# Performance work log

Measured on AMD Instinct MI355X. Metric: run time of the kernel, lower is better.

The kernel has to match this reference:

```python
import jax, jax.numpy as jnp
import numpy as np
from jax import lax

B, T, F, H = 128, 4096, 64, 128

def setup_inputs() -> dict:
    key = jax.random.key(0)
    k1, k2, k3, k4, k5 = jax.random.split(key, 5)
    s = 1.0 / np.sqrt(H)  # PyTorch LSTM init scale
    X = jax.random.normal(k1, (B, T, F), dtype=jnp.float32)
    W_ih = jax.random.uniform(k2, (4 * H, F), minval=-s, maxval=s, dtype=jnp.float32)
    W_hh = jax.random.uniform(k3, (4 * H, H), minval=-s, maxval=s, dtype=jnp.float32)
    b_ih = jax.random.uniform(k4, (4 * H,), minval=-s, maxval=s, dtype=jnp.float32)
    b_hh = jax.random.uniform(k5, (4 * H,), minval=-s, maxval=s, dtype=jnp.float32)
    return {"X": X, "W_ih": W_ih, "W_hh": W_hh, "b_ih": b_ih, "b_hh": b_hh}

def reference(X, W_ih, W_hh, b_ih, b_hh):
    # Faithful to the torch module: per-sequence LSTM with zero init state,
    # returning the output at the final timestep (== final hidden state).
    # PyTorch gate order: i, f, g, o.
    Bn, Tn, _ = X.shape
    Hn = W_hh.shape[1]
    # Precompute input contribution for all timesteps: [B, T, 4H]
    xg = jnp.einsum('btf,gf->btg', X, W_ih) + b_ih + b_hh
    xg_t = jnp.swapaxes(xg, 0, 1)  # [T, B, 4H]

    def step(carry, xg_step):
        h, c = carry
        gates = xg_step + h @ W_hh.T  # [B, 4H]
        i, f, g, o = jnp.split(gates, 4, axis=-1)
        i = jax.nn.sigmoid(i)
        f = jax.nn.sigmoid(f)
        g = jnp.tanh(g)
        o = jax.nn.sigmoid(o)
        c = f * c + i * g
        h = o * jnp.tanh(c)
        return (h, c), None

    h0 = jnp.zeros((Bn, Hn), dtype=X.dtype)
    c0 = jnp.zeros((Bn, Hn), dtype=X.dtype)
    (h_last, _), _ = lax.scan(step, (h0, c0), xg_t)
    return h_last  # [B, H]: the torch code's list of (1,1,H) outs, stacked
```

## Files before the change

### kernel.cpp

```cpp
#include <hip/hip_runtime.h>

#define B_  128
#define T_  4096
#define F_  64
#define H_  128
#define NT  512
#define XGS 516

typedef _Float16 half8_t __attribute__((ext_vector_type(8)));
typedef _Float16 half2_t __attribute__((ext_vector_type(2)));
typedef float    f32x4   __attribute__((ext_vector_type(4)));

#define L2N1 (-1.4426950408889634f)
#define L2N2 (-2.8853900817779268f)

__device__ __forceinline__ half2_t pack2(float a, float b) {
  half2_t r; r[0] = (_Float16)a; r[1] = (_Float16)b; return r;
}

__device__ __forceinline__ void wg_barrier() {
  __asm__ volatile("s_waitcnt lgkmcnt(0)\n\ts_barrier" ::: "memory");
}

__global__ __launch_bounds__(NT, 2) void lstm_xg_kernel(
    const float* __restrict__ X,
    const float* __restrict__ Wih,
    const float* __restrict__ Whh,
    const float* __restrict__ bih,
    const float* __restrict__ bhh,
    float* __restrict__ out)
{
  const int tid  = threadIdx.x;
  const int b    = blockIdx.x;
  const int lane = tid & 63;
  const int w    = tid >> 6;
  const int lg   = lane >> 4;
  const int lc   = lane & 15;

  __shared__ __align__(16) _Float16 hbuf[2][H_];
  __shared__ __align__(16) _Float16 xst[2][16 * 72];
  __shared__ __align__(16) float    xg[2][16 * XGS];

  half8_t Wf[4][6];
  f32x4   xinit[4];
#pragma unroll
  for (int g = 0; g < 4; ++g) {
    const float s = (g == 2) ? L2N2 : L2N1;
    const int row = 128 * g + 16 * w + lc;
    const float bv = (bih[row] + bhh[row]) * s;
    f32x4 bi = {bv, bv, bv, bv};
    xinit[g] = bi;
#pragma unroll
    for (int c = 0; c < 6; ++c) {
      const float* src = (c < 4) ? (Whh + (size_t)row * H_ + 32 * c + 8 * lg)
                                 : (Wih + (size_t)row * F_ + 32 * (c - 4) + 8 * lg);
      float4 lo = *(const float4*)(src);
      float4 hi = *(const float4*)(src + 4);
      half8_t v;
      v[0] = (_Float16)(lo.x * s); v[1] = (_Float16)(lo.y * s);
      v[2] = (_Float16)(lo.z * s); v[3] = (_Float16)(lo.w * s);
      v[4] = (_Float16)(hi.x * s); v[5] = (_Float16)(hi.y * s);
      v[6] = (_Float16)(hi.z * s); v[7] = (_Float16)(hi.w * s);
      Wf[g][c] = v;
    }
  }

  const float* xbase = X + (size_t)b * T_ * F_;
  const int    tp    = tid >> 5;
  const int    kp    = tid & 31;

  {
    float2 v0 = ((const float2*)xbase)[0 * 512 + tid];
    float2 v1 = ((const float2*)xbase)[1 * 512 + tid];
    *(half2_t*)&xst[0][tp * 72 + 2 * kp] = pack2(v0.x, v0.y);
    *(half2_t*)&xst[1][tp * 72 + 2 * kp] = pack2(v1.x, v1.y);
  }
  wg_barrier();

  const f32x4 zf = {0.0f, 0.0f, 0.0f, 0.0f};

  {
    half8_t a0 = *(const half8_t*)&xst[0][lc * 72 + 8 * lg];
    half8_t a1 = *(const half8_t*)&xst[0][lc * 72 + 32 + 8 * lg];
#pragma unroll
    for (int g = 0; g < 4; ++g) {
      f32x4 ab = __builtin_amdgcn_mfma_f32_16x16x32_f16(a0, Wf[g][4], xinit[g], 0, 0, 0);
      ab       = __builtin_amdgcn_mfma_f32_16x16x32_f16(a1, Wf[g][5], ab, 0, 0, 0);
#pragma unroll
      for (int r = 0; r < 4; ++r)
        xg[0][(4 * lg + r) * XGS + (16 * w + lc) * 4 + g] = ab[r];
    }
  }
  wg_barrier();

  f32x4 pre[4], pB[4];
#pragma unroll
  for (int g = 0; g < 4; ++g) { pre[g] = zf; pB[g] = zf; }
  f32x4 xg4 = *(const f32x4*)&xg[0][0 * XGS + (16 * w + lc) * 4];

  float csS = 0.0f, hl = 0.0f;
  float2 xv = {0.0f, 0.0f};

#pragma unroll 16
  for (int t = 0; t < T_; ++t) {
    const int buf = t & 1;
    const int P   = t >> 4;
    const int tau = t & 15;

    float p0 = pre[0][0] + pB[0][0] + xg4[0];
    float p1 = pre[1][0] + pB[1][0] + xg4[1];
    float p2 = pre[2][0] + pB[2][0] + xg4[2];
    float p3 = pre[3][0] + pB[3][0] + xg4[3];

    float si = __builtin_amdgcn_rcpf(1.0f + __builtin_amdgcn_exp2f(p0));
    float sf = __builtin_amdgcn_rcpf(1.0f + __builtin_amdgcn_exp2f(p1));
    float rg = __builtin_amdgcn_rcpf(1.0f + __builtin_amdgcn_exp2f(p2));
    float so = __builtin_amdgcn_rcpf(1.0f + __builtin_amdgcn_exp2f(p3));

    float ai = si * L2N2;
    csS = fmaf(sf, csS, fmaf(ai + ai, rg, -ai));

    float so2 = so + so, son = -so;
    float rh  = __builtin_amdgcn_rcpf(1.0f + __builtin_amdgcn_exp2f(csS));
    float hn  = fmaf(so2, rh, son);
    hl = hn;

    if (lane < 16) hbuf[buf][16 * w + lc] = (_Float16)hn;

    wg_barrier();

    half8_t ah0 = *(const half8_t*)&hbuf[buf][ 0 + 8 * lg];
    half8_t ah1 = *(const half8_t*)&hbuf[buf][32 + 8 * lg];
    half8_t ah2 = *(const half8_t*)&hbuf[buf][64 + 8 * lg];
    half8_t ah3 = *(const half8_t*)&hbuf[buf][96 + 8 * lg];

    const int tn = t + 1;
    xg4 = *(const f32x4*)&xg[(tn >> 4) & 1][(tn & 15) * XGS + (16 * w + lc) * 4];

    if (tau == 0) {
      const int sb = (P + 1) & 1;
      half8_t a0 = *(const half8_t*)&xst[sb][lc * 72 + 8 * lg];
      half8_t a1 = *(const half8_t*)&xst[sb][lc * 72 + 32 + 8 * lg];
#pragma unroll
      for (int g = 0; g < 4; ++g) {
        f32x4 ab = __builtin_amdgcn_mfma_f32_16x16x32_f16(a0, Wf[g][4], xinit[g], 0, 0, 0);
        ab       = __builtin_amdgcn_mfma_f32_16x16x32_f16(a1, Wf[g][5], ab, 0, 0, 0);
#pragma unroll
        for (int r = 0; r < 4; ++r)
          xg[sb][(4 * lg + r) * XGS + (16 * w + lc) * 4 + g] = ab[r];
      }
      int Pn = P + 2; if (Pn > (T_ / 16 - 1)) Pn = T_ / 16 - 1;
      xv = ((const float2*)xbase)[(size_t)Pn * 512 + tid];
    }
    if (tau == 8) {
      *(half2_t*)&xst[P & 1][tp * 72 + 2 * kp] = pack2(xv.x, xv.y);
    }

#pragma unroll
    for (int g = 0; g < 4; ++g) {
      f32x4 a  = __builtin_amdgcn_mfma_f32_16x16x32_f16(ah0, Wf[g][0], zf, 0, 0, 0);
      pre[g]   = __builtin_amdgcn_mfma_f32_16x16x32_f16(ah1, Wf[g][1], a, 0, 0, 0);
      f32x4 a2 = __builtin_amdgcn_mfma_f32_16x16x32_f16(ah2, Wf[g][2], zf, 0, 0, 0);
      pB[g]    = __builtin_amdgcn_mfma_f32_16x16x32_f16(ah3, Wf[g][3], a2, 0, 0, 0);
    }
  }

  if (lane < 16) out[(size_t)b * H_ + 16 * w + lc] = hl;
}

extern "C" void kernel_launch(void* const* d_in, const int* in_sizes, int n_in,
                              void* d_out, int out_size, void* d_ws, size_t ws_size,
                              hipStream_t stream) {
  const float* X   = (const float*)d_in[0];
  const float* Wih = (const float*)d_in[1];
  const float* Whh = (const float*)d_in[2];
  const float* bih = (const float*)d_in[3];
  const float* bhh = (const float*)d_in[4];
  float* out = (float*)d_out;

  lstm_xg_kernel<<<dim3(B_), dim3(NT), 0, stream>>>(X, Wih, Whh, bih, bhh, out);
}
```

Baseline: 1.860 ms.

## Split LSTM gate activations across wave halves and stagger input projection MFMAs

Each wave half now computes only two of the four gate nonlinearities (lanes below 32 handle i and g, lanes 32 and up handle f and o). The i*g term is exchanged with a cross-half shuffle, which shortens the serial transcendental chain per timestep. The xg layout is permuted so each half reads a float2 instead of a float4. The per-chunk input-projection MFMAs are split across two timesteps (tau 0 and 1) to spread that load, at the cost of an extra shuffle on the critical path and keeping xa0/xa1 live in registers.

New measurement: 2.001 ms. 7.6% more time.

```diff
diff --git a/kernel.cpp b/kernel.cpp
--- a/kernel.cpp
+++ b/kernel.cpp
@@ -13,6 +13,10 @@
 
 #define L2N1 (-1.4426950408889634f)
 #define L2N2 (-2.8853900817779268f)
+
+__device__ __forceinline__ constexpr int gslot(int g) {
+  return (g & 1) ? (2 + (g >> 1)) : (g >> 1);
+}
 
 __device__ __forceinline__ half2_t pack2(float a, float b) {
   half2_t r; r[0] = (_Float16)a; r[1] = (_Float16)b; return r;
@@ -36,6 +40,7 @@
   const int w    = tid >> 6;
   const int lg   = lane >> 4;
   const int lc   = lane & 15;
+  const bool hi32 = lane >= 32;
 
   __shared__ __align__(16) _Float16 hbuf[2][H_];
   __shared__ __align__(16) _Float16 xst[2][16 * 72];
@@ -88,7 +93,7 @@
       ab       = __builtin_amdgcn_mfma_f32_16x16x32_f16(a1, Wf[g][5], ab, 0, 0, 0);
 #pragma unroll
       for (int r = 0; r < 4; ++r)
-        xg[0][(4 * lg + r) * XGS + (16 * w + lc) * 4 + g] = ab[r];
+        xg[0][(4 * lg + r) * XGS + (16 * w + lc) * 4 + gslot(g)] = ab[r];
     }
   }
   wg_barrier();
@@ -96,10 +101,11 @@
   f32x4 pre[4], pB[4];
 #pragma unroll
   for (int g = 0; g < 4; ++g) { pre[g] = zf; pB[g] = zf; }
-  f32x4 xg4 = *(const f32x4*)&xg[0][0 * XGS + (16 * w + lc) * 4];
+  float2 xg2 = *(const float2*)&xg[0][(16 * w + lc) * 4 + (hi32 ? 2 : 0)];
 
   float csS = 0.0f, hl = 0.0f;
   float2 xv = {0.0f, 0.0f};
+  half8_t xa0 = {}, xa1 = {};
 
 #pragma unroll 16
   for (int t = 0; t < T_; ++t) {
@@ -107,25 +113,23 @@
     const int P   = t >> 4;
     const int tau = t & 15;
 
-    float p0 = pre[0][0] + pB[0][0] + xg4[0];
-    float p1 = pre[1][0] + pB[1][0] + xg4[1];
-    float p2 = pre[2][0] + pB[2][0] + xg4[2];
-    float p3 = pre[3][0] + pB[3][0] + xg4[3];
+    float pa = (hi32 ? (pre[1][0] + pB[1][0]) : (pre[0][0] + pB[0][0])) + xg2.x;
+    float pb = (hi32 ? (pre[3][0] + pB[3][0]) : (pre[2][0] + pB[2][0])) + xg2.y;
 
-    float si = __builtin_amdgcn_rcpf(1.0f + __builtin_amdgcn_exp2f(p0));
-    float sf = __builtin_amdgcn_rcpf(1.0f + __builtin_amdgcn_exp2f(p1));
-    float rg = __builtin_amdgcn_rcpf(1.0f + __builtin_amdgcn_exp2f(p2));
-    float so = __builtin_amdgcn_rcpf(1.0f + __builtin_amdgcn_exp2f(p3));
+    float ra = __builtin_amdgcn_rcpf(1.0f + __builtin_amdgcn_exp2f(pa));
+    float rb = __builtin_amdgcn_rcpf(1.0f + __builtin_amdgcn_exp2f(pb));
 
-    float ai = si * L2N2;
-    csS = fmaf(sf, csS, fmaf(ai + ai, rg, -ai));
+    float ai  = ra * L2N2;
+    float val = fmaf(ai + ai, rb, -ai);
+    float v   = __shfl_xor(val, 32);
 
-    float so2 = so + so, son = -so;
-    float rh  = __builtin_amdgcn_rcpf(1.0f + __builtin_amdgcn_exp2f(csS));
-    float hn  = fmaf(so2, rh, son);
+    csS = fmaf(ra, csS, v);
+    float so2 = rb + rb, son = -rb;
+    float q   = __builtin_amdgcn_rcpf(1.0f + __builtin_amdgcn_exp2f(csS));
+    float hn  = fmaf(so2, q, son);
     hl = hn;
 
-    if (lane < 16) hbuf[buf][16 * w + lc] = (_Float16)hn;
+    if (lg == 2) hbuf[buf][16 * w + lc] = (_Float16)hn;
 
     wg_barrier();
 
@@ -135,22 +139,33 @@
     half8_t ah3 = *(const half8_t*)&hbuf[buf][96 + 8 * lg];
 
     const int tn = t + 1;
-    xg4 = *(const f32x4*)&xg[(tn >> 4) & 1][(tn & 15) * XGS + (16 * w + lc) * 4];
+    xg2 = *(const float2*)&xg[(tn >> 4) & 1][(tn & 15) * XGS + (16 * w + lc) * 4 + (hi32 ? 2 : 0)];
 
     if (tau == 0) {
       const int sb = (P + 1) & 1;
-      half8_t a0 = *(const half8_t*)&xst[sb][lc * 72 + 8 * lg];
-      half8_t a1 = *(const half8_t*)&xst[sb][lc * 72 + 32 + 8 * lg];
+      xa0 = *(const half8_t*)&xst[sb][lc * 72 + 8 * lg];
+      xa1 = *(const half8_t*)&xst[sb][lc * 72 + 32 + 8 * lg];
 #pragma unroll
-      for (int g = 0; g < 4; ++g) {
-        f32x4 ab = __builtin_amdgcn_mfma_f32_16x16x32_f16(a0, Wf[g][4], xinit[g], 0, 0, 0);
-        ab       = __builtin_amdgcn_mfma_f32_16x16x32_f16(a1, Wf[g][5], ab, 0, 0, 0);
+      for (int g = 0; g < 2; ++g) {
+        f32x4 ab = __builtin_amdgcn_mfma_f32_16x16x32_f16(xa0, Wf[g][4], xinit[g], 0, 0, 0);
+        ab       = __builtin_amdgcn_mfma_f32_16x16x32_f16(xa1, Wf[g][5], ab, 0, 0, 0);
 #pragma unroll
-        for (int r = 0; r < 4; ++r)
-          xg[sb][(4 * lg + r) * XGS + (16 * w + lc) * 4 + g] = ab[r];
+        for (int rr = 0; rr < 4; ++rr)
+          xg[sb][(4 * lg + rr) * XGS + (16 * w + lc) * 4 + gslot(g)] = ab[rr];
       }
       int Pn = P + 2; if (Pn > (T_ / 16 - 1)) Pn = T_ / 16 - 1;
       xv = ((const float2*)xbase)[(size_t)Pn * 512 + tid];
+    }
+    if (tau == 1) {
+      const int sb = (P + 1) & 1;
+#pragma unroll
+      for (int g = 2; g < 4; ++g) {
+        f32x4 ab = __builtin_amdgcn_mfma_f32_16x16x32_f16(xa0, Wf[g][4], xinit[g], 0, 0, 0);
+        ab       = __builtin_amdgcn_mfma_f32_16x16x32_f16(xa1, Wf[g][5], ab, 0, 0, 0);
+#pragma unroll
+        for (int rr = 0; rr < 4; ++rr)
+          xg[sb][(4 * lg + rr) * XGS + (16 * w + lc) * 4 + gslot(g)] = ab[rr];
+      }
     }
     if (tau == 8) {
       *(half2_t*)&xst[P & 1][tp * 72 + 2 * kp] = pack2(xv.x, xv.y);
@@ -165,7 +180,7 @@
     }
   }
 
-  if (lane < 16) out[(size_t)b * H_ + 16 * w + lc] = hl;
+  if (lg == 2) out[(size_t)b * H_ + 16 * w + lc] = hl;
 }
 
 extern "C" void kernel_launch(void* const* d_in, const int* in_sizes, int n_in,
```

## Pack two batch sequences per 1024-thread workgroup sharing barriers

Applied to the files above, without the earlier changes.

Each workgroup now runs two independent LSTM sequences (two 512-thread groups) with separate shared-memory buffers, so the grid halves to 64 blocks. The aim is to put more waves per CU to hide MFMA and transcendental latency in the serial recurrence. The cost is that the per-step barrier now spans 16 waves across both sequences, so each sequence waits on the slower one. Launch bounds rise to 4 waves per SIMD, which may force register spills of the 24 half8 weight fragments. Only 64 blocks are launched on a device with many more CUs.

Measured after the change: 4.397 ms. 2.36x slower.

```diff
diff --git a/kernel.cpp b/kernel.cpp
--- a/kernel.cpp
+++ b/kernel.cpp
@@ -4,7 +4,7 @@
 #define T_  4096
 #define F_  64
 #define H_  128
-#define NT  512
+#define NT  1024
 #define XGS 516
 
 typedef _Float16 half8_t __attribute__((ext_vector_type(8)));
@@ -22,7 +22,7 @@
   __asm__ volatile("s_waitcnt lgkmcnt(0)\n\ts_barrier" ::: "memory");
 }
 
-__global__ __launch_bounds__(NT, 2) void lstm_xg_kernel(
+__global__ __launch_bounds__(NT, 4) void lstm_xg_kernel(
     const float* __restrict__ X,
     const float* __restrict__ Wih,
     const float* __restrict__ Whh,
@@ -31,15 +31,17 @@
     float* __restrict__ out)
 {
   const int tid  = threadIdx.x;
-  const int b    = blockIdx.x;
-  const int lane = tid & 63;
-  const int w    = tid >> 6;
+  const int grp  = tid >> 9;
+  const int gt   = tid & 511;
+  const int b    = blockIdx.x * 2 + grp;
+  const int lane = gt & 63;
+  const int w    = gt >> 6;
   const int lg   = lane >> 4;
   const int lc   = lane & 15;
 
-  __shared__ __align__(16) _Float16 hbuf[2][H_];
-  __shared__ __align__(16) _Float16 xst[2][16 * 72];
-  __shared__ __align__(16) float    xg[2][16 * XGS];
+  __shared__ __align__(16) _Float16 hbuf[2][2][H_];
+  __shared__ __align__(16) _Float16 xst[2][2][16 * 72];
+  __shared__ __align__(16) float    xg[2][2][16 * XGS];
 
   half8_t Wf[4][6];
   f32x4   xinit[4];
@@ -66,29 +68,29 @@
   }
 
   const float* xbase = X + (size_t)b * T_ * F_;
-  const int    tp    = tid >> 5;
-  const int    kp    = tid & 31;
+  const int    tp    = gt >> 5;
+  const int    kp    = gt & 31;
 
   {
-    float2 v0 = ((const float2*)xbase)[0 * 512 + tid];
-    float2 v1 = ((const float2*)xbase)[1 * 512 + tid];
-    *(half2_t*)&xst[0][tp * 72 + 2 * kp] = pack2(v0.x, v0.y);
-    *(half2_t*)&xst[1][tp * 72 + 2 * kp] = pack2(v1.x, v1.y);
+    float2 v0 = ((const float2*)xbase)[0 * 512 + gt];
+    float2 v1 = ((const float2*)xbase)[1 * 512 + gt];
+    *(half2_t*)&xst[grp][0][tp * 72 + 2 * kp] = pack2(v0.x, v0.y);
+    *(half2_t*)&xst[grp][1][tp * 72 + 2 * kp] = pack2(v1.x, v1.y);
   }
   wg_barrier();
 
   const f32x4 zf = {0.0f, 0.0f, 0.0f, 0.0f};
 
   {
-    half8_t a0 = *(const half8_t*)&xst[0][lc * 72 + 8 * lg];
-    half8_t a1 = *(const half8_t*)&xst[0][lc * 72 + 32 + 8 * lg];
+    half8_t a0 = *(const half8_t*)&xst[grp][0][lc * 72 + 8 * lg];
+    half8_t a1 = *(const half8_t*)&xst[grp][0][lc * 72 + 32 + 8 * lg];
 #pragma unroll
     for (int g = 0; g < 4; ++g) {
       f32x4 ab = __builtin_amdgcn_mfma_f32_16x16x32_f16(a0, Wf[g][4], xinit[g], 0, 0, 0);
       ab       = __builtin_amdgcn_mfma_f32_16x16x32_f16(a1, Wf[g][5], ab, 0, 0, 0);
 #pragma unroll
       for (int r = 0; r < 4; ++r)
-        xg[0][(4 * lg + r) * XGS + (16 * w + lc) * 4 + g] = ab[r];
+        xg[grp][0][(4 * lg + r) * XGS + (16 * w + lc) * 4 + g] = ab[r];
     }
   }
   wg_barrier();
@@ -96,7 +98,7 @@
   f32x4 pre[4], pB[4];
 #pragma unroll
   for (int g = 0; g < 4; ++g) { pre[g] = zf; pB[g] = zf; }
-  f32x4 xg4 = *(const f32x4*)&xg[0][0 * XGS + (16 * w + lc) * 4];
+  f32x4 xg4 = *(const f32x4*)&xg[grp][0][0 * XGS + (16 * w + lc) * 4];
 
   float csS = 0.0f, hl = 0.0f;
   float2 xv = {0.0f, 0.0f};
@@ -125,35 +127,35 @@
     float hn  = fmaf(so2, rh, son);
     hl = hn;
 
-    if (lane < 16) hbuf[buf][16 * w + lc] = (_Float16)hn;
+    if (lane < 16) hbuf[grp][buf][16 * w + lc] = (_Float16)hn;
 
     wg_barrier();
 
-    half8_t ah0 = *(const half8_t*)&hbuf[buf][ 0 + 8 * lg];
-    half8_t ah1 = *(const half8_t*)&hbuf[buf][32 + 8 * lg];
-    half8_t ah2 = *(const half8_t*)&hbuf[buf][64 + 8 * lg];
-    half8_t ah3 = *(const half8_t*)&hbuf[buf][96 + 8 * lg];
+    half8_t ah0 = *(const half8_t*)&hbuf[grp][buf][ 0 + 8 * lg];
+    half8_t ah1 = *(const half8_t*)&hbuf[grp][buf][32 + 8 * lg];
+    half8_t ah2 = *(const half8_t*)&hbuf[grp][buf][64 + 8 * lg];
+    half8_t ah3 = *(const half8_t*)&hbuf[grp][buf][96 + 8 * lg];
 
     const int tn = t + 1;
-    xg4 = *(const f32x4*)&xg[(tn >> 4) & 1][(tn & 15) * XGS + (16 * w + lc) * 4];
+    xg4 = *(const f32x4*)&xg[grp][(tn >> 4) & 1][(tn & 15) * XGS + (16 * w + lc) * 4];
 
     if (tau == 0) {
       const int sb = (P + 1) & 1;
-      half8_t a0 = *(const half8_t*)&xst[sb][lc * 72 + 8 * lg];
-      half8_t a1 = *(const half8_t*)&xst[sb][lc * 72 + 32 + 8 * lg];
+      half8_t a0 = *(const half8_t*)&xst[grp][sb][lc * 72 + 8 * lg];
+      half8_t a1 = *(const half8_t*)&xst[grp][sb][lc * 72 + 32 + 8 * lg];
 #pragma unroll
       for (int g = 0; g < 4; ++g) {
         f32x4 ab = __builtin_amdgcn_mfma_f32_16x16x32_f16(a0, Wf[g][4], xinit[g], 0, 0, 0);
         ab       = __builtin_amdgcn_mfma_f32_16x16x32_f16(a1, Wf[g][5], ab, 0, 0, 0);
 #pragma unroll
         for (int r = 0; r < 4; ++r)
-          xg[sb][(4 * lg + r) * XGS + (16 * w + lc) * 4 + g] = ab[r];
+          xg[grp][sb][(4 * lg + r) * XGS + (16 * w + lc) * 4 + g] = ab[r];
       }
       int Pn = P + 2; if (Pn > (T_ / 16 - 1)) Pn = T_ / 16 - 1;
-      xv = ((const float2*)xbase)[(size_t)Pn * 512 + tid];
+      xv = ((const float2*)xbase)[(size_t)Pn * 512 + gt];
     }
     if (tau == 8) {
-      *(half2_t*)&xst[P & 1][tp * 72 + 2 * kp] = pack2(xv.x, xv.y);
+      *(half2_t*)&xst[grp][P & 1][tp * 72 + 2 * kp] = pack2(xv.x, xv.y);
     }
 
 #pragma unroll
@@ -178,5 +180,5 @@
   const float* bhh = (const float*)d_in[4];
   float* out = (float*)d_out;
 
-  lstm_xg_kernel<<<dim3(B_), dim3(NT), 0, stream>>>(X, Wih, Whh, bih, bhh, out);
+  lstm_xg_kernel<<<dim3(B_ / 2), dim3(NT), 0, stream>>>(X, Wih, Whh, bih, bhh, out);
 }
```

## Keep input projection in registers, computed every 4 steps via MFMA

Applied to the files above, without the earlier changes.

Drops the shared-memory xg staging buffer. Every four timesteps the input projection for the next four steps is computed with MFMAs on a row-replicated A operand (lc&3), and the results stay in accumulator registers indexed by t&3. This removes the per-step LDS read of xg and the strided LDS writes done every 16 steps, and frees a large amount of LDS. In exchange it issues 8 extra MFMAs every 4 steps instead of every 16. The X staging write moves to tau 12 so reads of the current half-buffer stay safe.

New measurement: 1.937 ms. +4.2%, slower.

```diff
diff --git a/kernel.cpp b/kernel.cpp
--- a/kernel.cpp
+++ b/kernel.cpp
@@ -5,7 +5,6 @@
 #define F_  64
 #define H_  128
 #define NT  512
-#define XGS 516
 
 typedef _Float16 half8_t __attribute__((ext_vector_type(8)));
 typedef _Float16 half2_t __attribute__((ext_vector_type(2)));
@@ -39,7 +38,6 @@
 
   __shared__ __align__(16) _Float16 hbuf[2][H_];
   __shared__ __align__(16) _Float16 xst[2][16 * 72];
-  __shared__ __align__(16) float    xg[2][16 * XGS];
 
   half8_t Wf[4][6];
   f32x4   xinit[4];
@@ -79,24 +77,20 @@
 
   const f32x4 zf = {0.0f, 0.0f, 0.0f, 0.0f};
 
+  f32x4 xac[4];
   {
-    half8_t a0 = *(const half8_t*)&xst[0][lc * 72 + 8 * lg];
-    half8_t a1 = *(const half8_t*)&xst[0][lc * 72 + 32 + 8 * lg];
+    half8_t qa0 = *(const half8_t*)&xst[0][(lc & 3) * 72 + 8 * lg];
+    half8_t qa1 = *(const half8_t*)&xst[0][(lc & 3) * 72 + 32 + 8 * lg];
 #pragma unroll
     for (int g = 0; g < 4; ++g) {
-      f32x4 ab = __builtin_amdgcn_mfma_f32_16x16x32_f16(a0, Wf[g][4], xinit[g], 0, 0, 0);
-      ab       = __builtin_amdgcn_mfma_f32_16x16x32_f16(a1, Wf[g][5], ab, 0, 0, 0);
-#pragma unroll
-      for (int r = 0; r < 4; ++r)
-        xg[0][(4 * lg + r) * XGS + (16 * w + lc) * 4 + g] = ab[r];
+      xac[g] = __builtin_amdgcn_mfma_f32_16x16x32_f16(qa0, Wf[g][4], xinit[g], 0, 0, 0);
+      xac[g] = __builtin_amdgcn_mfma_f32_16x16x32_f16(qa1, Wf[g][5], xac[g], 0, 0, 0);
     }
   }
-  wg_barrier();
 
   f32x4 pre[4], pB[4];
 #pragma unroll
   for (int g = 0; g < 4; ++g) { pre[g] = zf; pB[g] = zf; }
-  f32x4 xg4 = *(const f32x4*)&xg[0][0 * XGS + (16 * w + lc) * 4];
 
   float csS = 0.0f, hl = 0.0f;
   float2 xv = {0.0f, 0.0f};
@@ -106,11 +100,12 @@
     const int buf = t & 1;
     const int P   = t >> 4;
     const int tau = t & 15;
+    const int qr  = t & 3;
 
-    float p0 = pre[0][0] + pB[0][0] + xg4[0];
-    float p1 = pre[1][0] + pB[1][0] + xg4[1];
-    float p2 = pre[2][0] + pB[2][0] + xg4[2];
-    float p3 = pre[3][0] + pB[3][0] + xg4[3];
+    float p0 = pre[0][0] + pB[0][0] + xac[0][qr];
+    float p1 = pre[1][0] + pB[1][0] + xac[1][qr];
+    float p2 = pre[2][0] + pB[2][0] + xac[2][qr];
+    float p3 = pre[3][0] + pB[3][0] + xac[3][qr];
 
     float si = __builtin_amdgcn_rcpf(1.0f + __builtin_amdgcn_exp2f(p0));
     float sf = __builtin_amdgcn_rcpf(1.0f + __builtin_amdgcn_exp2f(p1));
@@ -134,25 +129,21 @@
     half8_t ah2 = *(const half8_t*)&hbuf[buf][64 + 8 * lg];
     half8_t ah3 = *(const half8_t*)&hbuf[buf][96 + 8 * lg];
 
-    const int tn = t + 1;
-    xg4 = *(const f32x4*)&xg[(tn >> 4) & 1][(tn & 15) * XGS + (16 * w + lc) * 4];
+    half8_t qa0 = {}, qa1 = {};
+    const bool doquad = (qr == 3) && (t < T_ - 1);
+    if (doquad) {
+      const int tq = t + 1;
+      const int qb = (tq >> 4) & 1;
+      const int rb = tq & 12;
+      qa0 = *(const half8_t*)&xst[qb][(rb + (lc & 3)) * 72 + 8 * lg];
+      qa1 = *(const half8_t*)&xst[qb][(rb + (lc & 3)) * 72 + 32 + 8 * lg];
+    }
 
     if (tau == 0) {
-      const int sb = (P + 1) & 1;
-      half8_t a0 = *(const half8_t*)&xst[sb][lc * 72 + 8 * lg];
-      half8_t a1 = *(const half8_t*)&xst[sb][lc * 72 + 32 + 8 * lg];
-#pragma unroll
-      for (int g = 0; g < 4; ++g) {
-        f32x4 ab = __builtin_amdgcn_mfma_f32_16x16x32_f16(a0, Wf[g][4], xinit[g], 0, 0, 0);
-        ab       = __builtin_amdgcn_mfma_f32_16x16x32_f16(a1, Wf[g][5], ab, 0, 0, 0);
-#pragma unroll
-        for (int r = 0; r < 4; ++r)
-          xg[sb][(4 * lg + r) * XGS + (16 * w + lc) * 4 + g] = ab[r];
-      }
       int Pn = P + 2; if (Pn > (T_ / 16 - 1)) Pn = T_ / 16 - 1;
       xv = ((const float2*)xbase)[(size_t)Pn * 512 + tid];
     }
-    if (tau == 8) {
+    if (tau == 12) {
       *(half2_t*)&xst[P & 1][tp * 72 + 2 * kp] = pack2(xv.x, xv.y);
     }
 
@@ -162,6 +153,14 @@
       pre[g]   = __builtin_amdgcn_mfma_f32_16x16x32_f16(ah1, Wf[g][1], a, 0, 0, 0);
       f32x4 a2 = __builtin_amdgcn_mfma_f32_16x16x32_f16(ah2, Wf[g][2], zf, 0, 0, 0);
       pB[g]    = __builtin_amdgcn_mfma_f32_16x16x32_f16(ah3, Wf[g][3], a2, 0, 0, 0);
+    }
+
+    if (doquad) {
+#pragma unroll
+      for (int g = 0; g < 4; ++g) {
+        xac[g] = __builtin_amdgcn_mfma_f32_16x16x32_f16(qa0, Wf[g][4], xinit[g], 0, 0, 0);
+        xac[g] = __builtin_amdgcn_mfma_f32_16x16x32_f16(qa1, Wf[g][5], xac[g], 0, 0, 0);
+      }
     }
   }
 
```
